# Performance work log

Measured on AMD Instinct MI355X. Metric: run time of the kernel, lower is better.

## Reference

```python
import jax, jax.numpy as jnp
import numpy as np


def setup_inputs() -> dict:
    key = jax.random.key(0)
    ks = jax.random.split(key, 6)
    B, H, W, C = 4, 56, 56, 256
    NH, K = 8, 7
    return {
        "x": jax.random.normal(ks[0], (B, H, W, C), dtype=jnp.float32),
        "w_qkv": jax.random.normal(ks[1], (C, 3 * C), dtype=jnp.float32) * 0.02,
        "b_qkv": jax.random.normal(ks[2], (3 * C,), dtype=jnp.float32) * 0.02,
        "rpb": jax.random.normal(ks[3], (NH, K * K), dtype=jnp.float32) * 0.02,
        "w_proj": jax.random.normal(ks[4], (C, C), dtype=jnp.float32) * 0.02,
        "b_proj": jax.random.normal(ks[5], (C,), dtype=jnp.float32) * 0.02,
    }


def _window_stack(xp, H, W, ks):
    # xp: (B, H+2p, W+2p, nh, hd) zero-padded map.
    # Returns (B, H, W, nh, ks*ks, hd): each pixel's ks x ks neighborhood,
    # row-major (h offset outer, w offset inner) to match torch unfold order.
    return jnp.stack(
        [xp[:, i:i + H, j:j + W] for i in range(ks) for j in range(ks)],
        axis=-2,
    )


def reference(x, w_qkv, b_qkv, rpb, w_proj, b_proj):
    B, H, W, C = x.shape
    nh, ks2 = rpb.shape
    ks = int(np.sqrt(ks2) + 0.5)  # 7
    hd = C // nh
    scale = hd ** -0.5
    pad = ks // 2  # dilation == 1

    qkv = (x @ w_qkv + b_qkv).reshape(B, H, W, 3, nh, hd)
    q = qkv[..., 0, :, :] * scale        # (B,H,W,nh,hd)
    k = qkv[..., 1, :, :]
    v = qkv[..., 2, :, :]

    pads = ((0, 0), (pad, pad), (pad, pad), (0, 0), (0, 0))
    kw = _window_stack(jnp.pad(k, pads), H, W, ks)  # (B,H,W,nh,ks2,hd)
    vw = _window_stack(jnp.pad(v, pads), H, W, ks)

    # scores over each pixel's ks*ks neighbors (zero-padded borders kept,
    # matching the torch reference), plus relative position bias.
    attn = jnp.einsum("bhwnd,bhwnkd->bhwnk", q, kw) + rpb[None, None, None]
    attn = jax.nn.softmax(attn, axis=-1)
    out = jnp.einsum("bhwnk,bhwnkd->bhwnd", attn, vw).reshape(B, H, W, C)
    return out @ w_proj + b_proj
```

## Files before the change

### kernel.cpp

```cpp
#include <hip/hip_runtime.h>
#include <hip/hip_bf16.h>


using frag_ab = __attribute__((ext_vector_type(8))) short;
using f32x4   = __attribute__((ext_vector_type(4))) float;

typedef const __attribute__((address_space(1))) unsigned int* gas_u32;
typedef __attribute__((address_space(3))) unsigned int*       las_u32;

__device__ __forceinline__ void gl_lds16(const void* g, void* l) {
    __builtin_amdgcn_global_load_lds((gas_u32)g, (las_u32)l, 16, 0, 0);
}

__device__ __forceinline__ float bflo(unsigned int u) { return __uint_as_float(u << 16); }
__device__ __forceinline__ float bfhi(unsigned int u) { return __uint_as_float(u & 0xffff0000u); }

__global__ __launch_bounds__(256) void prep(
    const float* __restrict__ x,      __hip_bfloat16* __restrict__ xb,
    const float* __restrict__ w_qkv,  __hip_bfloat16* __restrict__ wqkvT,
    const float* __restrict__ w_proj, __hip_bfloat16* __restrict__ wprojT,
    __hip_bfloat16* __restrict__ kp,  __hip_bfloat16* __restrict__ vp)
{
    const int bid = blockIdx.x;
    const int tid = threadIdx.x;
    if (bid < 3136) {
        const int i = bid * 256 + tid;
        const float4 v = ((const float4*)x)[i];
        union { ushort4 u; __hip_bfloat16 h[4]; } o;
        o.h[0] = __float2bfloat16(v.x); o.h[1] = __float2bfloat16(v.y);
        o.h[2] = __float2bfloat16(v.z); o.h[3] = __float2bfloat16(v.w);
        ((ushort4*)xb)[i] = o.u;
    } else if (bid < 3904) {
        const int idx = (bid - 3136) * 256 + tid;
        const int k = idx & 255, n = idx >> 8;
        wqkvT[idx] = __float2bfloat16(w_qkv[k * 768 + n]);
    } else if (bid < 4160) {
        const int idx = (bid - 3904) * 256 + tid;
        const int k = idx & 255, n = idx >> 8;
        wprojT[idx] = __float2bfloat16(w_proj[k * 256 + n]);
    } else {
        const int u    = (bid - 4160) * 256 + tid;
        const int ip   = u / 30720;
        const int rem  = u - ip * 30720;
        const int cloc = rem >> 5;
        const int q16  = rem & 31;
        const int img  = ip >> 1;
        __hip_bfloat16* base = (ip & 1) ? vp : kp;
        int prow, pcol;
        if (cloc < 512) {
            const int r8 = cloc >> 6;
            prow = (r8 < 3) ? r8 : r8 + 56;
            pcol = cloc & 63;
        } else {
            const int c2 = cloc - 512;
            prow = 3 + (c2 >> 3);
            const int cc = c2 & 7;
            pcol = (cc < 3) ? cc : cc + 56;
        }
        *(uint4*)(base + (((size_t)(img * 64 + prow)) * 64 + pcol) * 256 + q16 * 8) =
            make_uint4(0u, 0u, 0u, 0u);
    }
}

#define GEMM128_BODY(EPILOGUE)                                                  \
    constexpr int K = 256;                                                      \
    __shared__ frag_ab As[8][64];                                     \
    __shared__ frag_ab Bs[8][64];                                     \
    const int tid  = threadIdx.x;                                               \
    const int lane = tid & 63;                                                  \
    const int w    = tid >> 6;                                                  \
    const int wm   = w >> 1, wn = w & 1;                                        \
    const int m0 = blockIdx.y * 128;                                            \
    const int n0 = blockIdx.x * 128;                                            \
    const int lrow = lane & 15;                                                 \
    const int lk   = (lane >> 4) * 8;                                           \
    const __hip_bfloat16* gA0 = A  + (size_t)(m0 + (2*w+0)*16 + lrow) * K + lk; \
    const __hip_bfloat16* gA1 = A  + (size_t)(m0 + (2*w+1)*16 + lrow) * K + lk; \
    const __hip_bfloat16* gB0 = BT + (size_t)(n0 + (2*w+0)*16 + lrow) * K + lk; \
    const __hip_bfloat16* gB1 = BT + (size_t)(n0 + (2*w+1)*16 + lrow) * K + lk; \
    f32x4 acc[4][4] = {};                                                       \
    for (int k0 = 0; k0 < K; k0 += 32) {                                        \
        gl_lds16(gA0 + k0, &As[2*w+0][0]);                                      \
        gl_lds16(gA1 + k0, &As[2*w+1][0]);                                      \
        gl_lds16(gB0 + k0, &Bs[2*w+0][0]);                                      \
        gl_lds16(gB1 + k0, &Bs[2*w+1][0]);                                      \
        __syncthreads();                                                        \
        frag_ab af[4], bf[4];                                                   \
        _Pragma("unroll")                                                       \
        for (int i = 0; i < 4; ++i) { af[i] = As[wm*4+i][lane]; bf[i] = Bs[wn*4+i][lane]; } \
        _Pragma("unroll")                                                       \
        for (int i = 0; i < 4; ++i)                                             \
            _Pragma("unroll")                                                   \
            for (int j = 0; j < 4; ++j)                                         \
                acc[i][j] = __builtin_amdgcn_mfma_f32_16x16x32_bf16(af[i], bf[j], acc[i][j], 0, 0, 0); \
        __syncthreads();                                                        \
    }                                                                           \
    const int rbase = (lane >> 4) * 4;                                          \
    const int cbase = lane & 15;                                                \
    _Pragma("unroll")                                                           \
    for (int fi = 0; fi < 4; ++fi) {                                            \
        const int rm = m0 + wm * 64 + fi * 16 + rbase;                          \
        _Pragma("unroll")                                                       \
        for (int fj = 0; fj < 4; ++fj) {                                        \
            const int cn = n0 + wn * 64 + fj * 16 + cbase;                      \
            const float bv = bias[cn];                                          \
            _Pragma("unroll")                                                   \
            for (int r = 0; r < 4; ++r) {                                       \
                const int m = rm + r;                                           \
                const float val = acc[fi][fj][r] + bv;                          \
                EPILOGUE                                                        \
            }                                                                   \
        }                                                                       \
    }

__global__ __launch_bounds__(256) void gemm_qkv(
    const __hip_bfloat16* __restrict__ A,
    const __hip_bfloat16* __restrict__ BT,
    const float* __restrict__ bias,
    float* __restrict__ qf,
    __hip_bfloat16* __restrict__ kp,
    __hip_bfloat16* __restrict__ vp,
    float qscale)
{
    GEMM128_BODY({
        const int sel = cn >> 8;
        if (sel == 0) {
            qf[(size_t)m * 256 + cn] = val * qscale;
        } else {
            const int c  = cn & 255;
            const int b  = m / 3136;
            const int r2 = m % 3136;
            const int yy = r2 / 56;
            const int xx = r2 % 56;
            __hip_bfloat16* dst = (sel == 1) ? kp : vp;
            dst[(((size_t)(b * 64 + yy + 3)) * 64 + (xx + 3)) * 256 + c] =
                __float2bfloat16(val);
        }
    })
}

__global__ __launch_bounds__(256) void gemm_proj(
    const __hip_bfloat16* __restrict__ A,
    const __hip_bfloat16* __restrict__ BT,
    const float* __restrict__ bias,
    float* __restrict__ C)
{
    GEMM128_BODY({
        C[(size_t)m * 256 + cn] = val;
    })
}

__global__ __launch_bounds__(64) void na2d_attn9(
    const float* __restrict__ qf,
    const __hip_bfloat16* __restrict__ kp,
    const __hip_bfloat16* __restrict__ vp,
    const float* __restrict__ rpb,
    __hip_bfloat16* __restrict__ out)
{
    const int lane = threadIdx.x;
    const int half = lane & 1;
    const int h    = (lane >> 1) & 7;
    const int tl   = (lane >> 4) & 3;

    const int bid = blockIdx.x;
    const int seg = (bid & 7) * 392 + (bid >> 3);
    const int row = seg / 14;
    const int x0  = (seg % 14) * 4;
    const int b   = row / 56;
    const int y   = row % 56;
    const int t   = row * 56 + x0 + tl;
    const int prow0 = b * 64 + y;

    __shared__ __hip_bfloat16 kbuf[10 * 264];
    __shared__ __hip_bfloat16 vbuf[10 * 264];
    __shared__ float srpb[8 * 49];

    for (int i = lane; i < 8 * 49; i += 64) srpb[i] = rpb[i];
    __syncthreads();

    float q[16];
    {
        const float4* qp = (const float4*)(qf + (size_t)t * 256 + h * 32 + half * 16);
        #pragma unroll
        for (int i = 0; i < 4; ++i) {
            const float4 v4 = qp[i];
            q[4 * i + 0] = v4.x; q[4 * i + 1] = v4.y;
            q[4 * i + 2] = v4.z; q[4 * i + 3] = v4.w;
        }
    }

    const int wroff = (lane >> 5) * 528 + (lane & 31) * 16;
    const int rdoff = tl * 528 + h * 64 + half * 32;

#define GLOAD(plane, ky, d0, d1, d2, d3, d4)                                    \
    do {                                                                        \
        const char* rb_ = (const char*)((plane) +                               \
            ((size_t)(prow0 + (ky)) * 64 + x0) * 256 + lane * 8);               \
        d0 = *(const uint4*)(rb_);                                              \
        d1 = *(const uint4*)(rb_ + 1024);                                       \
        d2 = *(const uint4*)(rb_ + 2048);                                       \
        d3 = *(const uint4*)(rb_ + 3072);                                       \
        d4 = *(const uint4*)(rb_ + 4096);                                       \
    } while (0)

#define LWRITE(buf, s0, s1, s2, s3, s4)                                         \
    do {                                                                        \
        char* wb_ = (char*)(buf) + wroff;                                       \
        *(uint4*)(wb_)        = s0;                                             \
        *(uint4*)(wb_ + 1056) = s1;                                             \
        *(uint4*)(wb_ + 2112) = s2;                                             \
        *(uint4*)(wb_ + 3168) = s3;                                             \
        *(uint4*)(wb_ + 4224) = s4;                                             \
    } while (0)

    const float* rp = &srpb[h * 49];
    float m = -1e30f, l = 0.f;
    float o[16] = {};

    uint4 k0, k1, k2, k3, k4, v0, v1, v2, v3, v4;
    GLOAD(kp, 0, k0, k1, k2, k3, k4);

    #pragma unroll 1
    for (int ky = 0; ky < 7; ++ky) {
        LWRITE(kbuf, k0, k1, k2, k3, k4);
        GLOAD(vp, ky, v0, v1, v2, v3, v4);
        float lg[7];
        #pragma unroll
        for (int kx = 0; kx < 7; ++kx) {
            const uint4* p = (const uint4*)((const char*)kbuf + rdoff + kx * 528);
            float s = 0.f;
            #pragma unroll
            for (int qd = 0; qd < 2; ++qd) {
                const uint4 wv = p[qd];
                const int o8 = qd * 8;
                s += q[o8 + 0] * bflo(wv.x) + q[o8 + 1] * bfhi(wv.x)
                   + q[o8 + 2] * bflo(wv.y) + q[o8 + 3] * bfhi(wv.y)
                   + q[o8 + 4] * bflo(wv.z) + q[o8 + 5] * bfhi(wv.z)
                   + q[o8 + 6] * bflo(wv.w) + q[o8 + 7] * bfhi(wv.w);
            }
            lg[kx] = s;
        }
        LWRITE(vbuf, v0, v1, v2, v3, v4);
        if (ky < 6) GLOAD(kp, ky + 1, k0, k1, k2, k3, k4);
        #pragma unroll
        for (int kx = 0; kx < 7; ++kx) {
            lg[kx] += __shfl_xor(lg[kx], 1, 64);
            lg[kx] += rp[ky * 7 + kx];
        }
        float rmax = lg[0];
        #pragma unroll
        for (int kx = 1; kx < 7; ++kx) rmax = fmaxf(rmax, lg[kx]);
        const float mnew  = fmaxf(m, rmax);
        const float alpha = __expf(m - mnew);
        m = mnew;
        l *= alpha;
        #pragma unroll
        for (int i = 0; i < 16; ++i) o[i] *= alpha;
        #pragma unroll
        for (int kx = 0; kx < 7; ++kx) {
            const float pr = __expf(lg[kx] - mnew);
            l += pr;
            const uint4* p = (const uint4*)((const char*)vbuf + rdoff + kx * 528);
            #pragma unroll
            for (int qd = 0; qd < 2; ++qd) {
                const uint4 wv = p[qd];
                const int o8 = qd * 8;
                o[o8 + 0] += pr * bflo(wv.x); o[o8 + 1] += pr * bfhi(wv.x);
                o[o8 + 2] += pr * bflo(wv.y); o[o8 + 3] += pr * bfhi(wv.y);
                o[o8 + 4] += pr * bflo(wv.z); o[o8 + 5] += pr * bfhi(wv.z);
                o[o8 + 6] += pr * bflo(wv.w); o[o8 + 7] += pr * bfhi(wv.w);
            }
        }
    }
#undef GLOAD
#undef LWRITE

    const float inv = 1.f / l;
    union { uint4 u[2]; __hip_bfloat16 hh[16]; } ob;
    #pragma unroll
    for (int i = 0; i < 16; ++i) ob.hh[i] = __float2bfloat16(o[i] * inv);
    uint4* op = (uint4*)(out + (size_t)t * 256 + h * 32 + half * 16);
    op[0] = ob.u[0];
    op[1] = ob.u[1];
}

extern "C" void kernel_launch(void* const* d_in, const int* in_sizes, int n_in,
                              void* d_out, int out_size, void* d_ws, size_t ws_size,
                              hipStream_t stream)
{
    const float* x      = (const float*)d_in[0];
    const float* w_qkv  = (const float*)d_in[1];
    const float* b_qkv  = (const float*)d_in[2];
    const float* rpb    = (const float*)d_in[3];
    const float* w_proj = (const float*)d_in[4];
    const float* b_proj = (const float*)d_in[5];
    float* out = (float*)d_out;

    const int M = 12544;

    char* wsp = (char*)d_ws;
    float* qf = (float*)wsp;                      wsp += (size_t)M * 256 * 4;
    __hip_bfloat16* kp    = (__hip_bfloat16*)wsp; wsp += (size_t)4 * 64 * 64 * 256 * 2;
    __hip_bfloat16* vp    = (__hip_bfloat16*)wsp; wsp += (size_t)4 * 64 * 64 * 256 * 2;
    __hip_bfloat16* xb    = (__hip_bfloat16*)wsp; wsp += (size_t)M * 256 * 2;
    __hip_bfloat16* attnb = (__hip_bfloat16*)wsp; wsp += (size_t)M * 256 * 2;
    __hip_bfloat16* wqkvT = (__hip_bfloat16*)wsp; wsp += (size_t)768 * 256 * 2;
    __hip_bfloat16* wprojT= (__hip_bfloat16*)wsp; wsp += (size_t)256 * 256 * 2;

    const float scale = 0.17677669529663689f;

    prep<<<5120, 256, 0, stream>>>(x, xb, w_qkv, wqkvT, w_proj, wprojT, kp, vp);

    gemm_qkv<<<dim3(6, 98), 256, 0, stream>>>(xb, wqkvT, b_qkv, qf, kp, vp, scale);

    na2d_attn9<<<3136, 64, 0, stream>>>(qf, kp, vp, rpb, attnb);

    gemm_proj<<<dim3(2, 98), 256, 0, stream>>>(attnb, wprojT, b_proj, out);
}
```

Baseline: 139.6 us.

## Load GEMM fragments directly to registers with double-buffered software pipeline

Replaces the LDS-staged GEMM (global_load_lds plus two barriers per k-step) with per-wave direct global loads of MFMA fragments into registers. Two register buffers are used so the loads for the next k-slices are issued while MFMAs run on the current ones. This removes LDS traffic and block-wide synchronization. In exchange, each A/B row is loaded redundantly by the two waves sharing it, and register pressure rises.

Result: slower. 151.1 us (+8.2%).

```diff
diff --git a/kernel.cpp b/kernel.cpp
--- a/kernel.cpp
+++ b/kernel.cpp
@@ -4,13 +4,6 @@
 
 using frag_ab = __attribute__((ext_vector_type(8))) short;
 using f32x4   = __attribute__((ext_vector_type(4))) float;
-
-typedef const __attribute__((address_space(1))) unsigned int* gas_u32;
-typedef __attribute__((address_space(3))) unsigned int*       las_u32;
-
-__device__ __forceinline__ void gl_lds16(const void* g, void* l) {
-    __builtin_amdgcn_global_load_lds((gas_u32)g, (las_u32)l, 16, 0, 0);
-}
 
 __device__ __forceinline__ float bflo(unsigned int u) { return __uint_as_float(u << 16); }
 __device__ __forceinline__ float bfhi(unsigned int u) { return __uint_as_float(u & 0xffff0000u); }
@@ -62,39 +55,66 @@
     }
 }
 
-#define GEMM128_BODY(EPILOGUE)                                                  \
+#define LOADF8(koff, A0, A1, A2, A3, B0, B1, B2, B3)                            \
+    do {                                                                        \
+        const char* pa_ = (const char*)gA + (size_t)(koff) * 2;                 \
+        const char* pb_ = (const char*)gB + (size_t)(koff) * 2;                 \
+        A0 = *(const frag_ab*)(pa_);                                            \
+        A1 = *(const frag_ab*)(pa_ + 8192);               \
+        A2 = *(const frag_ab*)(pa_ + 16384);                                    \
+        A3 = *(const frag_ab*)(pa_ + 24576);                                    \
+        B0 = *(const frag_ab*)(pb_);                                            \
+        B1 = *(const frag_ab*)(pb_ + 8192);                                     \
+        B2 = *(const frag_ab*)(pb_ + 16384);                                    \
+        B3 = *(const frag_ab*)(pb_ + 24576);                                    \
+    } while (0)
+
+#define MFMA16(A0, A1, A2, A3, B0, B1, B2, B3)                                  \
+    do {                                                                        \
+        acc[0][0] = __builtin_amdgcn_mfma_f32_16x16x32_bf16(A0, B0, acc[0][0], 0, 0, 0); \
+        acc[0][1] = __builtin_amdgcn_mfma_f32_16x16x32_bf16(A0, B1, acc[0][1], 0, 0, 0); \
+        acc[0][2] = __builtin_amdgcn_mfma_f32_16x16x32_bf16(A0, B2, acc[0][2], 0, 0, 0); \
+        acc[0][3] = __builtin_amdgcn_mfma_f32_16x16x32_bf16(A0, B3, acc[0][3], 0, 0, 0); \
+        acc[1][0] = __builtin_amdgcn_mfma_f32_16x16x32_bf16(A1, B0, acc[1][0], 0, 0, 0); \
+        acc[1][1] = __builtin_amdgcn_mfma_f32_16x16x32_bf16(A1, B1, acc[1][1], 0, 0, 0); \
+        acc[1][2] = __builtin_amdgcn_mfma_f32_16x16x32_bf16(A1, B2, acc[1][2], 0, 0, 0); \
+        acc[1][3] = __builtin_amdgcn_mfma_f32_16x16x32_bf16(A1, B3, acc[1][3], 0, 0, 0); \
+        acc[2][0] = __builtin_amdgcn_mfma_f32_16x16x32_bf16(A2, B0, acc[2][0], 0, 0, 0); \
+        acc[2][1] = __builtin_amdgcn_mfma_f32_16x16x32_bf16(A2, B1, acc[2][1], 0, 0, 0); \
+        acc[2][2] = __builtin_amdgcn_mfma_f32_16x16x32_bf16(A2, B2, acc[2][2], 0, 0, 0); \
+        acc[2][3] = __builtin_amdgcn_mfma_f32_16x16x32_bf16(A2, B3, acc[2][3], 0, 0, 0); \
+        acc[3][0] = __builtin_amdgcn_mfma_f32_16x16x32_bf16(A3, B0, acc[3][0], 0, 0, 0); \
+        acc[3][1] = __builtin_amdgcn_mfma_f32_16x16x32_bf16(A3, B1, acc[3][1], 0, 0, 0); \
+        acc[3][2] = __builtin_amdgcn_mfma_f32_16x16x32_bf16(A3, B2, acc[3][2], 0, 0, 0); \
+        acc[3][3] = __builtin_amdgcn_mfma_f32_16x16x32_bf16(A3, B3, acc[3][3], 0, 0, 0); \
+    } while (0)
+
+#define GEMM_DIRECT_BODY(EPILOGUE)                                              \
     constexpr int K = 256;                                                      \
-    __shared__ frag_ab As[8][64];                                     \
-    __shared__ frag_ab Bs[8][64];                                     \
     const int tid  = threadIdx.x;                                               \
     const int lane = tid & 63;                                                  \
     const int w    = tid >> 6;                                                  \
     const int wm   = w >> 1, wn = w & 1;                                        \
     const int m0 = blockIdx.y * 128;                                            \
     const int n0 = blockIdx.x * 128;                                            \
-    const int lrow = lane & 15;                                                 \
-    const int lk   = (lane >> 4) * 8;                                           \
-    const __hip_bfloat16* gA0 = A  + (size_t)(m0 + (2*w+0)*16 + lrow) * K + lk; \
-    const __hip_bfloat16* gA1 = A  + (size_t)(m0 + (2*w+1)*16 + lrow) * K + lk; \
-    const __hip_bfloat16* gB0 = BT + (size_t)(n0 + (2*w+0)*16 + lrow) * K + lk; \
-    const __hip_bfloat16* gB1 = BT + (size_t)(n0 + (2*w+1)*16 + lrow) * K + lk; \
+    const __hip_bfloat16* gA =                                                  \
+        A  + (size_t)(m0 + wm * 64 + (lane & 15)) * K + (lane >> 4) * 8;        \
+    const __hip_bfloat16* gB =                                                  \
+        BT + (size_t)(n0 + wn * 64 + (lane & 15)) * K + (lane >> 4) * 8;        \
     f32x4 acc[4][4] = {};                                                       \
-    for (int k0 = 0; k0 < K; k0 += 32) {                                        \
-        gl_lds16(gA0 + k0, &As[2*w+0][0]);                                      \
-        gl_lds16(gA1 + k0, &As[2*w+1][0]);                                      \
-        gl_lds16(gB0 + k0, &Bs[2*w+0][0]);                                      \
-        gl_lds16(gB1 + k0, &Bs[2*w+1][0]);                                      \
-        __syncthreads();                                                        \
-        frag_ab af[4], bf[4];                                                   \
-        _Pragma("unroll")                                                       \
-        for (int i = 0; i < 4; ++i) { af[i] = As[wm*4+i][lane]; bf[i] = Bs[wn*4+i][lane]; } \
-        _Pragma("unroll")                                                       \
-        for (int i = 0; i < 4; ++i)                                             \
-            _Pragma("unroll")                                                   \
-            for (int j = 0; j < 4; ++j)                                         \
-                acc[i][j] = __builtin_amdgcn_mfma_f32_16x16x32_bf16(af[i], bf[j], acc[i][j], 0, 0, 0); \
-        __syncthreads();                                                        \
+    frag_ab xa0, xa1, xa2, xa3, xb0, xb1, xb2, xb3;                \
+    frag_ab ya0, ya1, ya2, ya3, yb0, yb1, yb2, yb3;                \
+    LOADF8(0,  xa0, xa1, xa2, xa3, xb0, xb1, xb2, xb3);                         \
+    LOADF8(32, ya0, ya1, ya2, ya3, yb0, yb1, yb2, yb3);                         \
+    _Pragma("unroll 1")                                                         \
+    for (int kk = 0; kk < 3; ++kk) {                                            \
+        MFMA16(xa0, xa1, xa2, xa3, xb0, xb1, xb2, xb3);                         \
+        LOADF8(kk * 64 + 64, xa0, xa1, xa2, xa3, xb0, xb1, xb2, xb3);           \
+        MFMA16(ya0, ya1, ya2, ya3, yb0, yb1, yb2, yb3);                         \
+        LOADF8(kk * 64 + 96, ya0, ya1, ya2, ya3, yb0, yb1, yb2, yb3);           \
     }                                                                           \
+    MFMA16(xa0, xa1, xa2, xa3, xb0, xb1, xb2, xb3);                             \
+    MFMA16(ya0, ya1, ya2, ya3, yb0, yb1, yb2, yb3);                             \
     const int rbase = (lane >> 4) * 4;                                          \
     const int cbase = lane & 15;                                                \
     _Pragma("unroll")                                                           \
@@ -122,7 +142,7 @@
     __hip_bfloat16* __restrict__ vp,
     float qscale)
 {
-    GEMM128_BODY({
+    GEMM_DIRECT_BODY({
         const int sel = cn >> 8;
         if (sel == 0) {
             qf[(size_t)m * 256 + cn] = val * qscale;
@@ -145,7 +165,7 @@
     const float* __restrict__ bias,
     float* __restrict__ C)
 {
-    GEMM128_BODY({
+    GEMM_DIRECT_BODY({
         C[(size_t)m * 256 + cn] = val;
     })
 }
```
